# Kernel tuning notes

Hardware: AMD Instinct MI355X
Metric: run time of the kernel (lower is better)

## Reference

```python
import jax, jax.numpy as jnp
import numpy as np
from jax import lax

B, T, L = 32, 64, 1500        # flows, max packets per flow, packet length (MTU)
H, DC = 128, 100              # lstm hidden, cnn feature dim
KS, ST = 5, 3                 # conv kernel/stride
FLAT = 54 * 32                # conv output length 1500->499->165->54, 32 channels


def setup_inputs() -> dict:
    key = jax.random.key(0)
    ks = jax.random.split(key, 12)
    s = 0.05
    X = jax.random.normal(ks[0], (B, T, L), jnp.float32)
    lengths = jax.random.randint(ks[1], (B,), 1, T + 1, dtype=jnp.int32)
    conv1_w = jax.random.normal(ks[2], (128, 1, KS), jnp.float32) * s
    conv2_w = jax.random.normal(ks[3], (32, 128, KS), jnp.float32) * s
    conv3_w = jax.random.normal(ks[4], (32, 32, KS), jnp.float32) * s
    lin_w = jax.random.normal(ks[5], (DC, FLAT), jnp.float32) * s
    w_ih0 = jax.random.normal(ks[6], (4 * H, DC), jnp.float32) * s
    w_hh0 = jax.random.normal(ks[7], (4 * H, H), jnp.float32) * s
    w_ih1 = jax.random.normal(ks[8], (4 * H, H), jnp.float32) * s
    w_hh1 = jax.random.normal(ks[9], (4 * H, H), jnp.float32) * s
    fc1_w = jax.random.normal(ks[10], (10, H), jnp.float32) * s
    fc2_w = jax.random.normal(ks[11], (2, 10), jnp.float32) * s
    return {"X": X, "lengths": lengths, "conv1_w": conv1_w, "conv2_w": conv2_w,
            "conv3_w": conv3_w, "lin_w": lin_w, "w_ih0": w_ih0, "w_hh0": w_hh0,
            "w_ih1": w_ih1, "w_hh1": w_hh1, "fc1_w": fc1_w, "fc2_w": fc2_w}


def _conv(x, w):
    # x: [N, Cin, L], w: [Cout, Cin, K] -> valid conv, stride 3 (torch Conv1d semantics)
    return lax.conv_general_dilated(x, w, (ST,), 'VALID',
                                    dimension_numbers=('NCH', 'OIH', 'NCH'))


def _lstm_layer(xs, mask, w_ih, w_hh):
    # xs: [T, B, D]; mask: [T, B] (True = valid step); no biases (bias=False)
    Bn = xs.shape[1]
    h0 = jnp.zeros((Bn, H), xs.dtype)
    c0 = jnp.zeros((Bn, H), xs.dtype)

    def step(carry, inp):
        h, c = carry
        x_t, m_t = inp
        gates = x_t @ w_ih.T + h @ w_hh.T          # [B, 4H]
        i, f, g, o = jnp.split(gates, 4, axis=-1)  # torch gate order i,f,g,o
        i, f, o = jax.nn.sigmoid(i), jax.nn.sigmoid(f), jax.nn.sigmoid(o)
        g = jnp.tanh(g)
        c_new = f * c + i * g
        h_new = o * jnp.tanh(c_new)
        m = m_t[:, None]
        h = jnp.where(m, h_new, h)  # freeze state past each flow's length
        c = jnp.where(m, c_new, c)
        return (h, c), h

    (h_f, c_f), hs = lax.scan(step, (h0, c0), (xs, mask))
    return hs, h_f


def reference(X, lengths, conv1_w, conv2_w, conv3_w, lin_w,
              w_ih0, w_hh0, w_ih1, w_hh1, fc1_w, fc2_w):
    leaky = jax.nn.leaky_relu  # slope 0.01 matches torch default
    # ODCNN over every packet (batched over all B*T packets instead of python loops)
    x = X.reshape(B * T, 1, L)
    x = leaky(_conv(x, conv1_w))   # [BT, 128, 499]
    x = leaky(_conv(x, conv2_w))   # [BT, 32, 165]
    x = leaky(_conv(x, conv3_w))   # [BT, 32, 54]
    feats = x.reshape(B * T, FLAT) @ lin_w.T          # [BT, 100] (no activation)
    feats = feats.reshape(B, T, DC).transpose(1, 0, 2)  # [T, B, 100]
    mask = jnp.arange(T)[:, None] < lengths[None, :]     # [T, B]
    hs1, _ = _lstm_layer(feats, mask, w_ih0, w_hh0)
    _, h2 = _lstm_layer(hs1, mask, w_ih1, w_hh1)         # h at step len-1, top layer
    out = leaky(h2 @ fc1_w.T)
    out = leaky(out @ fc2_w.T)                           # [B, out_dim]
    return out
```

## Files before the change

### kernel.cpp

```cpp
#include <hip/hip_runtime.h>
#include <hip/hip_bf16.h>

#define B_ 32
#define T_ 64
#define H_ 128
#define L3OUT 54
#define FLAT_ 1728

typedef __attribute__((ext_vector_type(8))) short bf16x8;
typedef __attribute__((ext_vector_type(4))) float f32x4;

__device__ __forceinline__ float leakyf(float v) { return v > 0.f ? v : 0.01f * v; }
__device__ __forceinline__ float sigmoidf_(float v) { return 1.f / (1.f + expf(-v)); }
__device__ __forceinline__ unsigned int bf16rne(float v) {
  unsigned int b = __float_as_uint(v);
  return (b + 0x7FFFu + ((b >> 16) & 1u)) >> 16;
}
__device__ __forceinline__ bf16x8 ldb8(const unsigned short* p) {
  return *(const bf16x8*)p;
}

__global__ __launch_bounds__(256) void k_prep(
    const float* __restrict__ w1, const float* __restrict__ w2,
    const float* __restrict__ w3, const float* __restrict__ linw,
    const float* __restrict__ wih0, const float* __restrict__ whh0,
    const float* __restrict__ wih1, const float* __restrict__ whh1,
    unsigned short* __restrict__ w1eh, unsigned short* __restrict__ w1el,
    unsigned short* __restrict__ w2h, unsigned short* __restrict__ w2l,
    unsigned short* __restrict__ w3h, unsigned short* __restrict__ w3l,
    unsigned short* __restrict__ linwh, unsigned short* __restrict__ linwl,
    unsigned short* __restrict__ wih0h, unsigned short* __restrict__ wih0l,
    float* __restrict__ whh0T, float* __restrict__ wih1T,
    float* __restrict__ whh1T) {
  const int e = blockIdx.x * 256 + threadIdx.x;
  if (e >= 264960) {
    int e5 = e - 264960;
    int m = e5 >> 16, r = e5 & 65535;
    int k = r >> 9, j = r & 511;
    const float* src = (m == 0) ? whh0 : ((m == 1) ? wih1 : whh1);
    float* dst = (m == 0) ? whh0T : ((m == 1) ? wih1T : whh1T);
    dst[r] = src[j * 128 + k];
    return;
  }
  float v;
  unsigned short* dh;
  unsigned short* dl;
  int di;
  if (e < 20480) {
    int cc = e / 5120, rem = e - cc * 5120;
    int c2 = rem / 160, r = rem - c2 * 160;
    int tap = r >> 5, c1l = r & 31;
    v = w2[c2 * 640 + (cc * 32 + c1l) * 5 + tap];
    dh = w2h; dl = w2l; di = e;
  } else if (e < 25600) {
    int e2 = e - 20480;
    int c3 = e2 / 160, r = e2 - c3 * 160;
    int tap = r >> 5, c2 = r & 31;
    v = w3[c3 * 160 + c2 * 5 + tap];
    dh = w3h; dl = w3l; di = e2;
  } else if (e < 198400) {
    int e3 = e - 25600;
    v = linw[e3];
    dh = linwh; dl = linwl; di = e3;
  } else if (e < 263936) {
    int e4 = e - 198400;
    int g = e4 >> 7, k = e4 & 127;
    v = (k < 100) ? wih0[g * 100 + k] : 0.f;
    dh = wih0h; dl = wih0l; di = e4;
  } else {
    int i = e - 263936;
    int c1 = i >> 3, j = i & 7;
    v = (j < 5) ? w1[c1 * 5 + j] : 0.f;
    dh = w1eh; dl = w1el; di = i;
  }
  unsigned int hb = bf16rne(v);
  float hf = __uint_as_float(hb << 16);
  unsigned int lb = bf16rne(v - hf);
  dh[di] = (unsigned short)hb;
  dl[di] = (unsigned short)lb;
}

__global__ __launch_bounds__(512) void k_conv123(
    const float* __restrict__ X, const float* __restrict__ w1,
    const unsigned short* __restrict__ w2h, const unsigned short* __restrict__ w2l,
    const unsigned short* __restrict__ w3h, const unsigned short* __restrict__ w3l,
    unsigned short* __restrict__ s3g) {
  __shared__ __align__(16) float Xs[1504];
  __shared__ __align__(16) unsigned int AhU[10640];

  const int n = blockIdx.x;
  const int tid = threadIdx.x;
  const int lane = tid & 63;
  const int w = tid >> 6;
  const int l15 = lane & 15;
  const int cg = lane >> 4;

  const float* Xn = X + (size_t)n * 1500;
  for (int i = tid; i < 1500; i += 512) Xs[i] = Xn[i];
  if (tid < 4) Xs[1500 + tid] = 0.f;
  for (int i = tid; i < 640; i += 512) AhU[10000 + i] = 0u;
  __syncthreads();

  float x0 = 0.f, x1 = 0.f, x2 = 0.f, x3 = 0.f, x4 = 0.f;
  if (tid < 500) {
    const float* xp = Xs + 3 * tid;
    x0 = xp[0]; x1 = xp[1]; x2 = xp[2]; x3 = xp[3]; x4 = xp[4];
  }

  f32x4 acc2[2][2];
#pragma unroll
  for (int a = 0; a < 2; ++a)
#pragma unroll
    for (int m = 0; m < 2; ++m) acc2[a][m] = (f32x4){0.f, 0.f, 0.f, 0.f};

  for (int cc = 0; cc < 4; ++cc) {
    __syncthreads();
    if (tid < 500) {
      const float* wc = w1 + cc * 160;
      unsigned int rowbuf[16];
#pragma unroll
      for (int p = 0; p < 16; ++p) {
        const float* wa = wc + 10 * p;
        float vA = fmaf(x4, wa[4], fmaf(x3, wa[3], fmaf(x2, wa[2], fmaf(x1, wa[1], x0 * wa[0]))));
        float vB = fmaf(x4, wa[9], fmaf(x3, wa[8], fmaf(x2, wa[7], fmaf(x1, wa[6], x0 * wa[5]))));
        vA = fmaxf(vA, 0.01f * vA);
        vB = fmaxf(vB, 0.01f * vB);
        rowbuf[p] = bf16rne(vA) | (bf16rne(vB) << 16);
      }
#pragma unroll
      for (int q = 0; q < 4; ++q)
        *(uint4*)(&AhU[tid * 20 + 4 * q]) = *(uint4*)(&rowbuf[4 * q]);
    }
    __syncthreads();
    const unsigned short* w2hB = w2h + cc * 5120;
    const unsigned short* w2lB = w2l + cc * 5120;
#pragma unroll
    for (int tap = 0; tap < 5; ++tap) {
      const int wc = tap * 32 + cg * 8;
      bf16x8 ah0 = ldb8(w2hB + l15 * 160 + wc);
      bf16x8 ah1 = ldb8(w2hB + (l15 + 16) * 160 + wc);
      bf16x8 al0 = ldb8(w2lB + l15 * 160 + wc);
      bf16x8 al1 = ldb8(w2lB + (l15 + 16) * 160 + wc);
      {
        bf16x8 bfr = ldb8((const unsigned short*)AhU + (3 * (w * 16 + l15) + tap) * 40 + cg * 8);
        acc2[0][0] = __builtin_amdgcn_mfma_f32_16x16x32_bf16(ah0, bfr, acc2[0][0], 0, 0, 0);
        acc2[0][0] = __builtin_amdgcn_mfma_f32_16x16x32_bf16(al0, bfr, acc2[0][0], 0, 0, 0);
        acc2[0][1] = __builtin_amdgcn_mfma_f32_16x16x32_bf16(ah1, bfr, acc2[0][1], 0, 0, 0);
        acc2[0][1] = __builtin_amdgcn_mfma_f32_16x16x32_bf16(al1, bfr, acc2[0][1], 0, 0, 0);
      }
      if (w < 3) {
        int nt = 8 + w;
        bf16x8 bfr = ldb8((const unsigned short*)AhU + (3 * (nt * 16 + l15) + tap) * 40 + cg * 8);
        acc2[1][0] = __builtin_amdgcn_mfma_f32_16x16x32_bf16(ah0, bfr, acc2[1][0], 0, 0, 0);
        acc2[1][0] = __builtin_amdgcn_mfma_f32_16x16x32_bf16(al0, bfr, acc2[1][0], 0, 0, 0);
        acc2[1][1] = __builtin_amdgcn_mfma_f32_16x16x32_bf16(ah1, bfr, acc2[1][1], 0, 0, 0);
        acc2[1][1] = __builtin_amdgcn_mfma_f32_16x16x32_bf16(al1, bfr, acc2[1][1], 0, 0, 0);
      }
    }
  }
  __syncthreads();
  for (int i = tid; i < 400; i += 512) AhU[176 * 20 + i] = 0u;
#pragma unroll
  for (int nti = 0; nti < 2; ++nti) {
    int nt = (nti == 0) ? w : (8 + w);
    if (nti == 0 || w < 3) {
      int l2 = nt * 16 + l15;
#pragma unroll
      for (int mt = 0; mt < 2; ++mt) {
#pragma unroll
        for (int j = 0; j < 2; ++j) {
          float e0 = leakyf(acc2[nti][mt][2 * j]);
          float e1 = leakyf(acc2[nti][mt][2 * j + 1]);
          AhU[l2 * 20 + mt * 8 + cg * 2 + j] = bf16rne(e0) | (bf16rne(e1) << 16);
        }
      }
    }
  }
  __syncthreads();
  if (w < 4) {
    f32x4 a3[2];
    a3[0] = (f32x4){0.f, 0.f, 0.f, 0.f};
    a3[1] = (f32x4){0.f, 0.f, 0.f, 0.f};
#pragma unroll
    for (int tap = 0; tap < 5; ++tap) {
      const int wc = tap * 32 + cg * 8;
      bf16x8 wh0 = ldb8(w3h + l15 * 160 + wc);
      bf16x8 wh1 = ldb8(w3h + (l15 + 16) * 160 + wc);
      bf16x8 wl0 = ldb8(w3l + l15 * 160 + wc);
      bf16x8 wl1 = ldb8(w3l + (l15 + 16) * 160 + wc);
      bf16x8 bfr = ldb8((const unsigned short*)AhU + (3 * (w * 16 + l15) + tap) * 40 + cg * 8);
      a3[0] = __builtin_amdgcn_mfma_f32_16x16x32_bf16(wh0, bfr, a3[0], 0, 0, 0);
      a3[0] = __builtin_amdgcn_mfma_f32_16x16x32_bf16(wl0, bfr, a3[0], 0, 0, 0);
      a3[1] = __builtin_amdgcn_mfma_f32_16x16x32_bf16(wh1, bfr, a3[1], 0, 0, 0);
      a3[1] = __builtin_amdgcn_mfma_f32_16x16x32_bf16(wl1, bfr, a3[1], 0, 0, 0);
    }
    int l3 = w * 16 + l15;
    if (l3 < L3OUT) {
#pragma unroll
      for (int mt = 0; mt < 2; ++mt) {
#pragma unroll
        for (int r = 0; r < 4; ++r) {
          int c3 = mt * 16 + cg * 4 + r;
          s3g[(size_t)n * FLAT_ + c3 * L3OUT + l3] = (unsigned short)bf16rne(leakyf(a3[mt][r]));
        }
      }
    }
  }
}

__global__ __launch_bounds__(448) void k_gemm_fx(
    const unsigned short* __restrict__ s3g,
    const unsigned short* __restrict__ linwh, const unsigned short* __restrict__ linwl,
    const unsigned short* __restrict__ wih0h, const unsigned short* __restrict__ wih0l,
    float* __restrict__ xg0) {
  __shared__ __align__(16) unsigned short fehS[16][136];
  __shared__ __align__(16) unsigned short felS[16][136];

  const int m0 = blockIdx.x * 16;
  const int tid = threadIdx.x;
  const int lane = tid & 63;
  const int w = tid >> 6;
  const int l15 = lane & 15;
  const int cg = lane >> 4;

  if (tid < 192) {
    int r = tid / 12, c = tid - r * 12;
    ((unsigned int*)&fehS[r][112])[c] = 0u;
    ((unsigned int*)&felS[r][112])[c] = 0u;
  }

  int brow = w * 16 + l15;
  if (brow > 99) brow = 99;
  const unsigned short* ap = s3g + (size_t)(m0 + l15) * FLAT_ + cg * 8;
  const unsigned short* bhp = linwh + (size_t)brow * FLAT_ + cg * 8;
  const unsigned short* blp = linwl + (size_t)brow * FLAT_ + cg * 8;

  f32x4 acc = (f32x4){0.f, 0.f, 0.f, 0.f};
#pragma unroll 6
  for (int ks = 0; ks < 54; ++ks) {
    bf16x8 af = ldb8(ap + ks * 32);
    bf16x8 bh = ldb8(bhp + ks * 32);
    bf16x8 bl = ldb8(blp + ks * 32);
    acc = __builtin_amdgcn_mfma_f32_16x16x32_bf16(af, bh, acc, 0, 0, 0);
    acc = __builtin_amdgcn_mfma_f32_16x16x32_bf16(af, bl, acc, 0, 0, 0);
  }
  const int jcol = w * 16 + l15;
#pragma unroll
  for (int r = 0; r < 4; ++r) {
    float v = acc[r];
    unsigned int hb = bf16rne(v);
    float hf = __uint_as_float(hb << 16);
    unsigned int lb = bf16rne(v - hf);
    fehS[cg * 4 + r][jcol] = (unsigned short)hb;
    felS[cg * 4 + r][jcol] = (unsigned short)lb;
  }
  __syncthreads();

#pragma unroll
  for (int nt0 = 0; nt0 < 5; ++nt0) {
    int nt = w + 7 * nt0;
    if (nt < 32) {
      f32x4 a = (f32x4){0.f, 0.f, 0.f, 0.f};
#pragma unroll
      for (int ks = 0; ks < 4; ++ks) {
        bf16x8 ah = ldb8(&fehS[l15][ks * 32 + cg * 8]);
        bf16x8 al = ldb8(&felS[l15][ks * 32 + cg * 8]);
        int br = nt * 16 + l15;
        bf16x8 bh = ldb8(wih0h + (size_t)br * 128 + ks * 32 + cg * 8);
        bf16x8 bl = ldb8(wih0l + (size_t)br * 128 + ks * 32 + cg * 8);
        a = __builtin_amdgcn_mfma_f32_16x16x32_bf16(ah, bh, a, 0, 0, 0);
        a = __builtin_amdgcn_mfma_f32_16x16x32_bf16(ah, bl, a, 0, 0, 0);
        a = __builtin_amdgcn_mfma_f32_16x16x32_bf16(al, bh, a, 0, 0, 0);
      }
#pragma unroll
      for (int r = 0; r < 4; ++r)
        xg0[(size_t)(m0 + cg * 4 + r) * 512 + nt * 16 + l15] = a[r];
    }
  }
}

__global__ __launch_bounds__(512) void k_lstm0(
    const float* __restrict__ xg0, const float* __restrict__ whh0T,
    const int* __restrict__ lengths, float* __restrict__ hs1) {
  __shared__ __align__(16) float h0s[H_];
  __shared__ float ps[16 * 128];
  const int b = blockIdx.x;
  const int tid = threadIdx.x;
  const int ks = tid >> 7;
  const int jj = tid & 127;
  float w[4][32];
#pragma unroll
  for (int kk = 0; kk < 32; ++kk) {
#pragma unroll
    for (int q = 0; q < 4; ++q)
      w[q][kk] = whh0T[(ks * 32 + kk) * 512 + q * 128 + jj];
  }
  if (tid < H_) h0s[tid] = 0.f;
  float c = 0.f;
  const int len = lengths[b];
  float xq0 = 0.f, xq1 = 0.f, xq2 = 0.f, xq3 = 0.f;
  if (tid < H_) {
    const float* xp = xg0 + (size_t)(b * T_) * 512;
    xq0 = xp[jj]; xq1 = xp[128 + jj]; xq2 = xp[256 + jj]; xq3 = xp[384 + jj];
  }
  __syncthreads();
  for (int t = 0; t < len; ++t) {
    float p0 = 0.f, p1 = 0.f, p2 = 0.f, p3 = 0.f;
#pragma unroll
    for (int k4 = 0; k4 < 8; ++k4) {
      float4 hv = *(const float4*)(h0s + ks * 32 + k4 * 4);
      p0 = fmaf(hv.x, w[0][k4 * 4], fmaf(hv.y, w[0][k4 * 4 + 1], fmaf(hv.z, w[0][k4 * 4 + 2], fmaf(hv.w, w[0][k4 * 4 + 3], p0))));
      p1 = fmaf(hv.x, w[1][k4 * 4], fmaf(hv.y, w[1][k4 * 4 + 1], fmaf(hv.z, w[1][k4 * 4 + 2], fmaf(hv.w, w[1][k4 * 4 + 3], p1))));
      p2 = fmaf(hv.x, w[2][k4 * 4], fmaf(hv.y, w[2][k4 * 4 + 1], fmaf(hv.z, w[2][k4 * 4 + 2], fmaf(hv.w, w[2][k4 * 4 + 3], p2))));
      p3 = fmaf(hv.x, w[3][k4 * 4], fmaf(hv.y, w[3][k4 * 4 + 1], fmaf(hv.z, w[3][k4 * 4 + 2], fmaf(hv.w, w[3][k4 * 4 + 3], p3))));
    }
    ps[(ks * 4 + 0) * 128 + jj] = p0;
    ps[(ks * 4 + 1) * 128 + jj] = p1;
    ps[(ks * 4 + 2) * 128 + jj] = p2;
    ps[(ks * 4 + 3) * 128 + jj] = p3;
    __syncthreads();
    if (tid < H_) {
      float gi = xq0 + ((ps[0 * 128 + jj] + ps[4 * 128 + jj]) + (ps[8 * 128 + jj] + ps[12 * 128 + jj]));
      float gf = xq1 + ((ps[1 * 128 + jj] + ps[5 * 128 + jj]) + (ps[9 * 128 + jj] + ps[13 * 128 + jj]));
      float gg = xq2 + ((ps[2 * 128 + jj] + ps[6 * 128 + jj]) + (ps[10 * 128 + jj] + ps[14 * 128 + jj]));
      float go = xq3 + ((ps[3 * 128 + jj] + ps[7 * 128 + jj]) + (ps[11 * 128 + jj] + ps[15 * 128 + jj]));
      float ig = sigmoidf_(gi);
      float fg = sigmoidf_(gf);
      float gt = tanhf(gg);
      float og = sigmoidf_(go);
      c = fg * c + ig * gt;
      float hn = og * tanhf(c);
      h0s[jj] = hn;
      hs1[((size_t)(b * T_ + t)) * H_ + jj] = hn;
      if (t + 1 < len) {
        const float* xp = xg0 + (size_t)(b * T_ + t + 1) * 512;
        xq0 = xp[jj]; xq1 = xp[128 + jj]; xq2 = xp[256 + jj]; xq3 = xp[384 + jj];
      }
    }
    __syncthreads();
  }
}

__global__ __launch_bounds__(512) void k_xg1(
    const float* __restrict__ hs1, const float* __restrict__ wih1T,
    float* __restrict__ xg1) {
  __shared__ __align__(16) float hsS[8][128];
  const int r0 = blockIdx.x * 8;
  const int tid = threadIdx.x;
  for (int i = tid; i < 8 * 128; i += 512) ((float*)hsS)[i] = hs1[(size_t)r0 * 128 + i];
  __syncthreads();
  float acc[8] = {0.f, 0.f, 0.f, 0.f, 0.f, 0.f, 0.f, 0.f};
#pragma unroll 4
  for (int k4 = 0; k4 < 32; ++k4) {
    float w0 = wih1T[(4 * k4 + 0) * 512 + tid];
    float w1v = wih1T[(4 * k4 + 1) * 512 + tid];
    float w2v = wih1T[(4 * k4 + 2) * 512 + tid];
    float w3v = wih1T[(4 * k4 + 3) * 512 + tid];
#pragma unroll
    for (int i = 0; i < 8; ++i) {
      float4 h = *(const float4*)(&hsS[i][4 * k4]);
      acc[i] += h.x * w0 + h.y * w1v + h.z * w2v + h.w * w3v;
    }
  }
#pragma unroll
  for (int i = 0; i < 8; ++i) xg1[((size_t)(r0 + i)) * 512 + tid] = acc[i];
}

__global__ __launch_bounds__(512) void k_lstm1(
    const float* __restrict__ xg1, const float* __restrict__ whh1T,
    const float* __restrict__ fc1, const float* __restrict__ fc2,
    const int* __restrict__ lengths, float* __restrict__ out) {
  __shared__ __align__(16) float h1s[H_];
  __shared__ float ps[16 * 128];
  __shared__ float tmp10[10];
  const int b = blockIdx.x;
  const int tid = threadIdx.x;
  const int ks = tid >> 7;
  const int jj = tid & 127;
  float w[4][32];
#pragma unroll
  for (int kk = 0; kk < 32; ++kk) {
#pragma unroll
    for (int q = 0; q < 4; ++q)
      w[q][kk] = whh1T[(ks * 32 + kk) * 512 + q * 128 + jj];
  }
  if (tid < H_) h1s[tid] = 0.f;
  float c = 0.f;
  const int len = lengths[b];
  float xq0 = 0.f, xq1 = 0.f, xq2 = 0.f, xq3 = 0.f;
  if (tid < H_) {
    const float* xp = xg1 + (size_t)(b * T_) * 512;
    xq0 = xp[jj]; xq1 = xp[128 + jj]; xq2 = xp[256 + jj]; xq3 = xp[384 + jj];
  }
  __syncthreads();
  for (int t = 0; t < len; ++t) {
    float p0 = 0.f, p1 = 0.f, p2 = 0.f, p3 = 0.f;
#pragma unroll
    for (int k4 = 0; k4 < 8; ++k4) {
      float4 hv = *(const float4*)(h1s + ks * 32 + k4 * 4);
      p0 = fmaf(hv.x, w[0][k4 * 4], fmaf(hv.y, w[0][k4 * 4 + 1], fmaf(hv.z, w[0][k4 * 4 + 2], fmaf(hv.w, w[0][k4 * 4 + 3], p0))));
      p1 = fmaf(hv.x, w[1][k4 * 4], fmaf(hv.y, w[1][k4 * 4 + 1], fmaf(hv.z, w[1][k4 * 4 + 2], fmaf(hv.w, w[1][k4 * 4 + 3], p1))));
      p2 = fmaf(hv.x, w[2][k4 * 4], fmaf(hv.y, w[2][k4 * 4 + 1], fmaf(hv.z, w[2][k4 * 4 + 2], fmaf(hv.w, w[2][k4 * 4 + 3], p2))));
      p3 = fmaf(hv.x, w[3][k4 * 4], fmaf(hv.y, w[3][k4 * 4 + 1], fmaf(hv.z, w[3][k4 * 4 + 2], fmaf(hv.w, w[3][k4 * 4 + 3], p3))));
    }
    ps[(ks * 4 + 0) * 128 + jj] = p0;
    ps[(ks * 4 + 1) * 128 + jj] = p1;
    ps[(ks * 4 + 2) * 128 + jj] = p2;
    ps[(ks * 4 + 3) * 128 + jj] = p3;
    __syncthreads();
    if (tid < H_) {
      float gi = xq0 + ((ps[0 * 128 + jj] + ps[4 * 128 + jj]) + (ps[8 * 128 + jj] + ps[12 * 128 + jj]));
      float gf = xq1 + ((ps[1 * 128 + jj] + ps[5 * 128 + jj]) + (ps[9 * 128 + jj] + ps[13 * 128 + jj]));
      float gg = xq2 + ((ps[2 * 128 + jj] + ps[6 * 128 + jj]) + (ps[10 * 128 + jj] + ps[14 * 128 + jj]));
      float go = xq3 + ((ps[3 * 128 + jj] + ps[7 * 128 + jj]) + (ps[11 * 128 + jj] + ps[15 * 128 + jj]));
      float ig = sigmoidf_(gi);
      float fg = sigmoidf_(gf);
      float gt = tanhf(gg);
      float og = sigmoidf_(go);
      c = fg * c + ig * gt;
      float hn = og * tanhf(c);
      h1s[jj] = hn;
      if (t + 1 < len) {
        const float* xp = xg1 + (size_t)(b * T_ + t + 1) * 512;
        xq0 = xp[jj]; xq1 = xp[128 + jj]; xq2 = xp[256 + jj]; xq3 = xp[384 + jj];
      }
    }
    __syncthreads();
  }
  if (tid < 10) {
    const float* fr = fc1 + tid * H_;
    float s = 0.f;
#pragma unroll 4
    for (int k = 0; k < H_; ++k) s += h1s[k] * fr[k];
    tmp10[tid] = leakyf(s);
  }
  __syncthreads();
  if (tid < 2) {
    const float* fr = fc2 + tid * 10;
    float s = 0.f;
#pragma unroll
    for (int j = 0; j < 10; ++j) s += tmp10[j] * fr[j];
    out[b * 2 + tid] = leakyf(s);
  }
}

extern "C" void kernel_launch(void* const* d_in, const int* in_sizes, int n_in,
                              void* d_out, int out_size, void* d_ws, size_t ws_size,
                              hipStream_t stream) {
  const float* X = (const float*)d_in[0];
  const int* lengths = (const int*)d_in[1];
  const float* w1 = (const float*)d_in[2];
  const float* w2 = (const float*)d_in[3];
  const float* w3 = (const float*)d_in[4];
  const float* linw = (const float*)d_in[5];
  const float* wih0 = (const float*)d_in[6];
  const float* whh0 = (const float*)d_in[7];
  const float* wih1 = (const float*)d_in[8];
  const float* whh1 = (const float*)d_in[9];
  const float* fc1 = (const float*)d_in[10];
  const float* fc2 = (const float*)d_in[11];

  char* wsb = (char*)d_ws;
  size_t off = 0;
  auto alloc = [&](size_t bytes) {
    char* p = wsb + off;
    off += (bytes + 511) & ~(size_t)511;
    return p;
  };
  unsigned short* s3g = (unsigned short*)alloc(2048 * 1728 * 2);
  float* xg0 = (float*)alloc(2048 * 512 * 4);
  unsigned short* w1eh = (unsigned short*)alloc(1024 * 2);
  unsigned short* w1el = (unsigned short*)alloc(1024 * 2);
  unsigned short* w2h = (unsigned short*)alloc(20480 * 2);
  unsigned short* w2l = (unsigned short*)alloc(20480 * 2);
  unsigned short* w3h = (unsigned short*)alloc(5120 * 2);
  unsigned short* w3l = (unsigned short*)alloc(5120 * 2);
  unsigned short* linwh = (unsigned short*)alloc(172800 * 2);
  unsigned short* linwl = (unsigned short*)alloc(172800 * 2);
  unsigned short* wih0h = (unsigned short*)alloc(65536 * 2);
  unsigned short* wih0l = (unsigned short*)alloc(65536 * 2);
  float* whh0T = (float*)alloc(65536 * 4);
  float* wih1T = (float*)alloc(65536 * 4);
  float* whh1T = (float*)alloc(65536 * 4);
  float* hs1 = (float*)alloc(262144 * 4);
  float* xg1 = (float*)alloc(2048 * 512 * 4);

  k_prep<<<1803, 256, 0, stream>>>(w1, w2, w3, linw, wih0, whh0, wih1, whh1,
                                   w1eh, w1el, w2h, w2l, w3h, w3l,
                                   linwh, linwl, wih0h, wih0l,
                                   whh0T, wih1T, whh1T);
  k_conv123<<<2048, 512, 0, stream>>>(X, w1, w2h, w2l, w3h, w3l, s3g);
  k_gemm_fx<<<128, 448, 0, stream>>>(s3g, linwh, linwl, wih0h, wih0l, xg0);
  k_lstm0<<<32, 512, 0, stream>>>(xg0, whh0T, lengths, hs1);
  k_xg1<<<256, 512, 0, stream>>>(hs1, wih1T, xg1);
  k_lstm1<<<32, 512, 0, stream>>>(xg1, whh1T, fc1, fc2, lengths, (float*)d_out);
}
```

Baseline: 284.2 us.

## Split conv kernel per packet into two halo-overlapped halves and spread LSTM input-gate loads

The fused conv1-3 kernel now launches two blocks per packet, each covering half of the conv3 output positions. The halves use overlapping input windows (halo recompute), which shrinks shared memory and improves occupancy and wave balance. In both LSTM recurrence kernels, the precomputed input-gate values are loaded by all 512 threads, one per gate element, and prefetched one step ahead. They are folded into the partial sums, so the 128 gate threads no longer issue four dependent global loads on the critical path. The cost is some redundant conv1/conv2 work in the overlap region and a larger grid.

```diff
diff --git a/kernel.cpp b/kernel.cpp
--- a/kernel.cpp
+++ b/kernel.cpp
@@ -80,42 +80,38 @@
   dl[di] = (unsigned short)lb;
 }
 
-__global__ __launch_bounds__(512) void k_conv123(
+__global__ __launch_bounds__(448) void k_conv123(
     const float* __restrict__ X, const float* __restrict__ w1,
     const unsigned short* __restrict__ w2h, const unsigned short* __restrict__ w2l,
     const unsigned short* __restrict__ w3h, const unsigned short* __restrict__ w3l,
     unsigned short* __restrict__ s3g) {
-  __shared__ __align__(16) float Xs[1504];
-  __shared__ __align__(16) unsigned int AhU[10640];
-
-  const int n = blockIdx.x;
+  __shared__ __align__(16) float Xs[1024];
+  __shared__ __align__(16) unsigned int AhU[352 * 20];
+
+  const int h = blockIdx.x;
+  const int n = blockIdx.y;
   const int tid = threadIdx.x;
   const int lane = tid & 63;
   const int w = tid >> 6;
   const int l15 = lane & 15;
   const int cg = lane >> 4;
-
-  const float* Xn = X + (size_t)n * 1500;
-  for (int i = tid; i < 1500; i += 512) Xs[i] = Xn[i];
-  if (tid < 4) Xs[1500 + tid] = 0.f;
-  for (int i = tid; i < 640; i += 512) AhU[10000 + i] = 0u;
-  __syncthreads();
-
-  float x0 = 0.f, x1 = 0.f, x2 = 0.f, x3 = 0.f, x4 = 0.f;
-  if (tid < 500) {
-    const float* xp = Xs + 3 * tid;
-    x0 = xp[0]; x1 = xp[1]; x2 = xp[2]; x3 = xp[3]; x4 = xp[4];
-  }
-
-  f32x4 acc2[2][2];
-#pragma unroll
-  for (int a = 0; a < 2; ++a)
-#pragma unroll
-    for (int m = 0; m < 2; ++m) acc2[a][m] = (f32x4){0.f, 0.f, 0.f, 0.f};
+  const int NPOS = h ? 212 : 338;
+  const int NT2 = h ? 5 : 7;
+
+  const float* Xn = X + (size_t)n * 1500 + 864 * h;
+  for (int i = tid; i < 1024; i += 448)
+    Xs[i] = (864 * h + i < 1500) ? Xn[i] : 0.f;
+  for (int i = tid + NPOS * 20; i < 7040; i += 448) AhU[i] = 0u;
+
+  f32x4 acc2[2];
+  acc2[0] = (f32x4){0.f, 0.f, 0.f, 0.f};
+  acc2[1] = (f32x4){0.f, 0.f, 0.f, 0.f};
 
   for (int cc = 0; cc < 4; ++cc) {
     __syncthreads();
-    if (tid < 500) {
+    if (tid < NPOS) {
+      const float* xp = Xs + 3 * tid;
+      float x0 = xp[0], x1 = xp[1], x2 = xp[2], x3 = xp[3], x4 = xp[4];
       const float* wc = w1 + cc * 160;
       unsigned int rowbuf[16];
 #pragma unroll
@@ -132,52 +128,43 @@
         *(uint4*)(&AhU[tid * 20 + 4 * q]) = *(uint4*)(&rowbuf[4 * q]);
     }
     __syncthreads();
-    const unsigned short* w2hB = w2h + cc * 5120;
-    const unsigned short* w2lB = w2l + cc * 5120;
-#pragma unroll
-    for (int tap = 0; tap < 5; ++tap) {
-      const int wc = tap * 32 + cg * 8;
-      bf16x8 ah0 = ldb8(w2hB + l15 * 160 + wc);
-      bf16x8 ah1 = ldb8(w2hB + (l15 + 16) * 160 + wc);
-      bf16x8 al0 = ldb8(w2lB + l15 * 160 + wc);
-      bf16x8 al1 = ldb8(w2lB + (l15 + 16) * 160 + wc);
-      {
-        bf16x8 bfr = ldb8((const unsigned short*)AhU + (3 * (w * 16 + l15) + tap) * 40 + cg * 8);
-        acc2[0][0] = __builtin_amdgcn_mfma_f32_16x16x32_bf16(ah0, bfr, acc2[0][0], 0, 0, 0);
-        acc2[0][0] = __builtin_amdgcn_mfma_f32_16x16x32_bf16(al0, bfr, acc2[0][0], 0, 0, 0);
-        acc2[0][1] = __builtin_amdgcn_mfma_f32_16x16x32_bf16(ah1, bfr, acc2[0][1], 0, 0, 0);
-        acc2[0][1] = __builtin_amdgcn_mfma_f32_16x16x32_bf16(al1, bfr, acc2[0][1], 0, 0, 0);
+    if (w < NT2) {
+      const unsigned short* w2hB = w2h + cc * 5120;
+      const unsigned short* w2lB = w2l + cc * 5120;
+#pragma unroll
+      for (int tap = 0; tap < 5; ++tap) {
+        const int wc = tap * 32 + cg * 8;
+        bf16x8 ah0 = ldb8(w2hB + l15 * 160 + wc);
+        bf16x8 ah1 = ldb8(w2hB + (l15 + 16) * 160 + wc);
+        bf16x8 al0 = ldb8(w2lB + l15 * 160 + wc);
+        bf16x8 al1 = ldb8(w2lB + (l15 + 16) * 160 + wc);
+        int row = 48 * w + 3 * l15 + tap;
+        bf16x8 bfr = ldb8((const unsigned short*)AhU + row * 40 + cg * 8);
+        acc2[0] = __builtin_amdgcn_mfma_f32_16x16x32_bf16(ah0, bfr, acc2[0], 0, 0, 0);
+        acc2[0] = __builtin_amdgcn_mfma_f32_16x16x32_bf16(al0, bfr, acc2[0], 0, 0, 0);
+        acc2[1] = __builtin_amdgcn_mfma_f32_16x16x32_bf16(ah1, bfr, acc2[1], 0, 0, 0);
+        acc2[1] = __builtin_amdgcn_mfma_f32_16x16x32_bf16(al1, bfr, acc2[1], 0, 0, 0);
       }
-      if (w < 3) {
-        int nt = 8 + w;
-        bf16x8 bfr = ldb8((const unsigned short*)AhU + (3 * (nt * 16 + l15) + tap) * 40 + cg * 8);
-        acc2[1][0] = __builtin_amdgcn_mfma_f32_16x16x32_bf16(ah0, bfr, acc2[1][0], 0, 0, 0);
-        acc2[1][0] = __builtin_amdgcn_mfma_f32_16x16x32_bf16(al0, bfr, acc2[1][0], 0, 0, 0);
-        acc2[1][1] = __builtin_amdgcn_mfma_f32_16x16x32_bf16(ah1, bfr, acc2[1][1], 0, 0, 0);
-        acc2[1][1] = __builtin_amdgcn_mfma_f32_16x16x32_bf16(al1, bfr, acc2[1][1], 0, 0, 0);
+    }
+  }
+  __syncthreads();
+  if (h) {
+    for (int i = tid; i < 380; i += 448) AhU[1600 + i] = 0u;
+  }
+  if (w < NT2) {
+    int l2l = 16 * w + l15;
+#pragma unroll
+    for (int mt = 0; mt < 2; ++mt) {
+#pragma unroll
+      for (int j = 0; j < 2; ++j) {
+        float e0 = leakyf(acc2[mt][2 * j]);
+        float e1 = leakyf(acc2[mt][2 * j + 1]);
+        AhU[l2l * 20 + mt * 8 + cg * 2 + j] = bf16rne(e0) | (bf16rne(e1) << 16);
       }
     }
   }
   __syncthreads();
-  for (int i = tid; i < 400; i += 512) AhU[176 * 20 + i] = 0u;
-#pragma unroll
-  for (int nti = 0; nti < 2; ++nti) {
-    int nt = (nti == 0) ? w : (8 + w);
-    if (nti == 0 || w < 3) {
-      int l2 = nt * 16 + l15;
-#pragma unroll
-      for (int mt = 0; mt < 2; ++mt) {
-#pragma unroll
-        for (int j = 0; j < 2; ++j) {
-          float e0 = leakyf(acc2[nti][mt][2 * j]);
-          float e1 = leakyf(acc2[nti][mt][2 * j + 1]);
-          AhU[l2 * 20 + mt * 8 + cg * 2 + j] = bf16rne(e0) | (bf16rne(e1) << 16);
-        }
-      }
-    }
-  }
-  __syncthreads();
-  if (w < 4) {
+  if (w < 2) {
     f32x4 a3[2];
     a3[0] = (f32x4){0.f, 0.f, 0.f, 0.f};
     a3[1] = (f32x4){0.f, 0.f, 0.f, 0.f};
@@ -188,13 +175,14 @@
       bf16x8 wh1 = ldb8(w3h + (l15 + 16) * 160 + wc);
       bf16x8 wl0 = ldb8(w3l + l15 * 160 + wc);
       bf16x8 wl1 = ldb8(w3l + (l15 + 16) * 160 + wc);
-      bf16x8 bfr = ldb8((const unsigned short*)AhU + (3 * (w * 16 + l15) + tap) * 40 + cg * 8);
+      int row = 48 * w + 3 * l15 + tap;
+      bf16x8 bfr = ldb8((const unsigned short*)AhU + row * 40 + cg * 8);
       a3[0] = __builtin_amdgcn_mfma_f32_16x16x32_bf16(wh0, bfr, a3[0], 0, 0, 0);
       a3[0] = __builtin_amdgcn_mfma_f32_16x16x32_bf16(wl0, bfr, a3[0], 0, 0, 0);
       a3[1] = __builtin_amdgcn_mfma_f32_16x16x32_bf16(wh1, bfr, a3[1], 0, 0, 0);
       a3[1] = __builtin_amdgcn_mfma_f32_16x16x32_bf16(wl1, bfr, a3[1], 0, 0, 0);
     }
-    int l3 = w * 16 + l15;
+    int l3 = 32 * h + 16 * w + l15;
     if (l3 < L3OUT) {
 #pragma unroll
       for (int mt = 0; mt < 2; ++mt) {
@@ -298,13 +286,10 @@
   if (tid < H_) h0s[tid] = 0.f;
   float c = 0.f;
   const int len = lengths[b];
-  float xq0 = 0.f, xq1 = 0.f, xq2 = 0.f, xq3 = 0.f;
-  if (tid < H_) {
-    const float* xp = xg0 + (size_t)(b * T_) * 512;
-    xq0 = xp[jj]; xq1 = xp[128 + jj]; xq2 = xp[256 + jj]; xq3 = xp[384 + jj];
-  }
+  float xcur = xg0[(size_t)(b * T_) * 512 + tid];
   __syncthreads();
   for (int t = 0; t < len; ++t) {
+    float xnxt = (t + 1 < len) ? xg0[(size_t)(b * T_ + t + 1) * 512 + tid] : 0.f;
     float p0 = 0.f, p1 = 0.f, p2 = 0.f, p3 = 0.f;
 #pragma unroll
     for (int k4 = 0; k4 < 8; ++k4) {
@@ -314,16 +299,20 @@
       p2 = fmaf(hv.x, w[2][k4 * 4], fmaf(hv.y, w[2][k4 * 4 + 1], fmaf(hv.z, w[2][k4 * 4 + 2], fmaf(hv.w, w[2][k4 * 4 + 3], p2))));
       p3 = fmaf(hv.x, w[3][k4 * 4], fmaf(hv.y, w[3][k4 * 4 + 1], fmaf(hv.z, w[3][k4 * 4 + 2], fmaf(hv.w, w[3][k4 * 4 + 3], p3))));
     }
+    p0 += (ks == 0) ? xcur : 0.f;
+    p1 += (ks == 1) ? xcur : 0.f;
+    p2 += (ks == 2) ? xcur : 0.f;
+    p3 += (ks == 3) ? xcur : 0.f;
     ps[(ks * 4 + 0) * 128 + jj] = p0;
     ps[(ks * 4 + 1) * 128 + jj] = p1;
     ps[(ks * 4 + 2) * 128 + jj] = p2;
     ps[(ks * 4 + 3) * 128 + jj] = p3;
     __syncthreads();
     if (tid < H_) {
-      float gi = xq0 + ((ps[0 * 128 + jj] + ps[4 * 128 + jj]) + (ps[8 * 128 + jj] + ps[12 * 128 + jj]));
-      float gf = xq1 + ((ps[1 * 128 + jj] + ps[5 * 128 + jj]) + (ps[9 * 128 + jj] + ps[13 * 128 + jj]));
-      float gg = xq2 + ((ps[2 * 128 + jj] + ps[6 * 128 + jj]) + (ps[10 * 128 + jj] + ps[14 * 128 + jj]));
-      float go = xq3 + ((ps[3 * 128 + jj] + ps[7 * 128 + jj]) + (ps[11 * 128 + jj] + ps[15 * 128 + jj]));
+      float gi = (ps[0 * 128 + jj] + ps[4 * 128 + jj]) + (ps[8 * 128 + jj] + ps[12 * 128 + jj]);
+      float gf = (ps[1 * 128 + jj] + ps[5 * 128 + jj]) + (ps[9 * 128 + jj] + ps[13 * 128 + jj]);
+      float gg = (ps[2 * 128 + jj] + ps[6 * 128 + jj]) + (ps[10 * 128 + jj] + ps[14 * 128 + jj]);
+      float go = (ps[3 * 128 + jj] + ps[7 * 128 + jj]) + (ps[11 * 128 + jj] + ps[15 * 128 + jj]);
       float ig = sigmoidf_(gi);
       float fg = sigmoidf_(gf);
       float gt = tanhf(gg);
@@ -332,12 +321,9 @@
       float hn = og * tanhf(c);
       h0s[jj] = hn;
       hs1[((size_t)(b * T_ + t)) * H_ + jj] = hn;
-      if (t + 1 < len) {
-        const float* xp = xg0 + (size_t)(b * T_ + t + 1) * 512;
-        xq0 = xp[jj]; xq1 = xp[128 + jj]; xq2 = xp[256 + jj]; xq3 = xp[384 + jj];
-      }
-    }
-    __syncthreads();
+    }
+    __syncthreads();
+    xcur = xnxt;
   }
 }
 
@@ -387,13 +373,10 @@
   if (tid < H_) h1s[tid] = 0.f;
   float c = 0.f;
   const int len = lengths[b];
-  float xq0 = 0.f, xq1 = 0.f, xq2 = 0.f, xq3 = 0.f;
-  if (tid < H_) {
-    const float* xp = xg1 + (size_t)(b * T_) * 512;
-    xq0 = xp[jj]; xq1 = xp[128 + jj]; xq2 = xp[256 + jj]; xq3 = xp[384 + jj];
-  }
+  float xcur = xg1[(size_t)(b * T_) * 512 + tid];
   __syncthreads();
   for (int t = 0; t < len; ++t) {
+    float xnxt = (t + 1 < len) ? xg1[(size_t)(b * T_ + t + 1) * 512 + tid] : 0.f;
     float p0 = 0.f, p1 = 0.f, p2 = 0.f, p3 = 0.f;
 #pragma unroll
     for (int k4 = 0; k4 < 8; ++k4) {
@@ -403,16 +386,20 @@
       p2 = fmaf(hv.x, w[2][k4 * 4], fmaf(hv.y, w[2][k4 * 4 + 1], fmaf(hv.z, w[2][k4 * 4 + 2], fmaf(hv.w, w[2][k4 * 4 + 3], p2))));
       p3 = fmaf(hv.x, w[3][k4 * 4], fmaf(hv.y, w[3][k4 * 4 + 1], fmaf(hv.z, w[3][k4 * 4 + 2], fmaf(hv.w, w[3][k4 * 4 + 3], p3))));
     }
+    p0 += (ks == 0) ? xcur : 0.f;
+    p1 += (ks == 1) ? xcur : 0.f;
+    p2 += (ks == 2) ? xcur : 0.f;
+    p3 += (ks == 3) ? xcur : 0.f;
     ps[(ks * 4 + 0) * 128 + jj] = p0;
     ps[(ks * 4 + 1) * 128 + jj] = p1;
     ps[(ks * 4 + 2) * 128 + jj] = p2;
     ps[(ks * 4 + 3) * 128 + jj] = p3;
     __syncthreads();
     if (tid < H_) {
-      float gi = xq0 + ((ps[0 * 128 + jj] + ps[4 * 128 + jj]) + (ps[8 * 128 + jj] + ps[12 * 128 + jj]));
-      float gf = xq1 + ((ps[1 * 128 + jj] + ps[5 * 128 + jj]) + (ps[9 * 128 + jj] + ps[13 * 128 + jj]));
-      float gg = xq2 + ((ps[2 * 128 + jj] + ps[6 * 128 + jj]) + (ps[10 * 128 + jj] + ps[14 * 128 + jj]));
-      float go = xq3 + ((ps[3 * 128 + jj] + ps[7 * 128 + jj]) + (ps[11 * 128 + jj] + ps[15 * 128 + jj]));
+      float gi = (ps[0 * 128 + jj] + ps[4 * 128 + jj]) + (ps[8 * 128 + jj] + ps[12 * 128 + jj]);
+      float gf = (ps[1 * 128 + jj] + ps[5 * 128 + jj]) + (ps[9 * 128 + jj] + ps[13 * 128 + jj]);
+      float gg = (ps[2 * 128 + jj] + ps[6 * 128 + jj]) + (ps[10 * 128 + jj] + ps[14 * 128 + jj]);
+      float go = (ps[3 * 128 + jj] + ps[7 * 128 + jj]) + (ps[11 * 128 + jj] + ps[15 * 128 + jj]);
       float ig = sigmoidf_(gi);
       float fg = sigmoidf_(gf);
       float gt = tanhf(gg);
@@ -420,12 +407,9 @@
       c = fg * c + ig * gt;
       float hn = og * tanhf(c);
       h1s[jj] = hn;
-      if (t + 1 < len) {
-        const float* xp = xg1 + (size_t)(b * T_ + t + 1) * 512;
-        xq0 = xp[jj]; xq1 = xp[128 + jj]; xq2 = xp[256 + jj]; xq3 = xp[384 + jj];
-      }
-    }
-    __syncthreads();
+    }
+    __syncthreads();
+    xcur = xnxt;
   }
   if (tid < 10) {
     const float* fr = fc1 + tid * H_;
@@ -489,7 +473,7 @@
                                    w1eh, w1el, w2h, w2l, w3h, w3l,
                                    linwh, linwl, wih0h, wih0l,
                                    whh0T, wih1T, whh1T);
-  k_conv123<<<2048, 512, 0, stream>>>(X, w1, w2h, w2l, w3h, w3l, s3g);
+  k_conv123<<<dim3(2, 2048), 448, 0, stream>>>(X, w1, w2h, w2l, w3h, w3l, s3g);
   k_gemm_fx<<<128, 448, 0, stream>>>(s3g, linwh, linwl, wih0h, wih0l, xg0);
   k_lstm0<<<32, 512, 0, stream>>>(xg0, whh0T, lengths, hs1);
   k_xg1<<<256, 512, 0, stream>>>(hs1, wih1T, xg1);
```

Measured after the change: 353.4 us. +24.4%, slower.
